# Optimization experiments

Hardware: AMD Instinct MI355X
Metric: run time of the kernel (lower is better)

Reference implementation:

```python
import jax, jax.numpy as jnp
import numpy as np

E, N, F = 50000, 25000, 32

def setup_inputs() -> dict:
    key = jax.random.key(0)
    ks = jax.random.split(key, 8)
    efeat = jax.random.normal(ks[0], (E, F), dtype=jnp.float32) * 0.2
    initial_efeats = jax.random.normal(ks[1], (E, F), dtype=jnp.float32) * 0.2
    # msg_fn / attn_fn: Linear(F, F*F)
    Wm = jax.random.normal(ks[2], (F * F, F), dtype=jnp.float32) * 0.05
    bm = jnp.zeros((F * F,), dtype=jnp.float32)
    Wa = jax.random.normal(ks[3], (F * F, F), dtype=jnp.float32) * 0.05
    ba = jnp.zeros((F * F,), dtype=jnp.float32)
    src = jax.random.randint(ks[4], (E,), 0, N, dtype=jnp.int32)
    dst = jax.random.randint(ks[5], (E,), 0, N, dtype=jnp.int32)
    return {"efeat": efeat, "initial_efeats": initial_efeats, "Wm": Wm, "bm": bm,
            "Wa": Wa, "ba": ba, "src": src, "dst": dst, "num_nodes": N}

def reference(efeat, initial_efeats, Wm, bm, Wa, ba, src, dst, num_nodes):
    e, f = efeat.shape
    # edge-conditioned transform matrices: [E, F, F]
    w_m = (efeat @ Wm.T + bm).reshape(e, f, f)
    w_a = (efeat @ Wa.T + ba).reshape(e, f, f)
    h = efeat[:, :, None]                 # [E, F, 1]
    ih = initial_efeats[:, :, None]       # [E, F, 1]
    e1 = w_m * h                          # [E, F, F]
    exp_e2 = jnp.exp(w_a * h)             # [E, F, F]
    initial_e1 = w_m * ih
    exp_initial_e2 = jnp.exp(w_a * ih)
    # scatter-sum exp weights to destination nodes, gather back at src
    sum_exp_node = jax.ops.segment_sum(exp_e2, dst, num_segments=num_nodes)  # [N, F, F]
    sum_exp = sum_exp_node[src] - exp_e2 + exp_initial_e2
    h1 = exp_e2 * e1
    initial_h1 = exp_initial_e2 * initial_e1
    m_node = jax.ops.segment_sum(h1, dst, num_segments=num_nodes)            # [N, F, F]
    h2 = (m_node[src] - h1 + initial_h1) / sum_exp
    return h2.sum(axis=1)                 # [E, F]
```

## Files before the change

### kernel.cpp

```cpp
#include <hip/hip_runtime.h>
#include <hip/hip_fp16.h>
#include <math.h>
#include <stdint.h>


#define FDIM   32
#define NNODES 25000
#define NPB    8

typedef __attribute__((ext_vector_type(8))) short bf16x8;
typedef __attribute__((ext_vector_type(4))) float f32x4;

__device__ __forceinline__ unsigned short f2bf(float f) {
    unsigned u = __float_as_uint(f);
    return (unsigned short)((u + 0x7FFFu + ((u >> 16) & 1u)) >> 16);
}
__device__ __forceinline__ unsigned f2e5(float f) {
    unsigned short hb = __half_as_ushort(__float2half(f));
    return (unsigned)((unsigned short)((hb + 0x7Fu + ((hb >> 8) & 1u)) >> 8)) & 0xFFu;
}
__device__ __forceinline__ float e52f(unsigned b) {
    return __half2float(__ushort_as_half((unsigned short)(b << 8)));
}

__global__ __launch_bounds__(256) void zero_f4(float4* __restrict__ p, int n4) {
    int i = blockIdx.x * blockDim.x + threadIdx.x;
    int stride = gridDim.x * blockDim.x;
    float4 z = make_float4(0.f, 0.f, 0.f, 0.f);
    for (; i < n4; i += stride) p[i] = z;
}

__global__ __launch_bounds__(256) void k_hist(
    const int* __restrict__ src, const int* __restrict__ dst,
    int* __restrict__ cnt_src, int* __restrict__ cnt_dst, int E) {
    int e = blockIdx.x * blockDim.x + threadIdx.x;
    if (e < E) {
        atomicAdd(&cnt_dst[dst[e]], 1);
        atomicAdd(&cnt_src[src[e]], 1);
    }
}

__global__ __launch_bounds__(256) void k_scan2(
    const int* __restrict__ cnt_dst, int* __restrict__ off_dst, int* __restrict__ cur_dst,
    const int* __restrict__ cnt_src, int* __restrict__ off_src, int* __restrict__ cur_src,
    int n) {
    const int* cnt = blockIdx.x ? cnt_src : cnt_dst;
    int* off = blockIdx.x ? off_src : off_dst;
    int* cur = blockIdx.x ? cur_src : cur_dst;
    __shared__ int wsum[4];
    __shared__ int carry_sh;
    const int tid = threadIdx.x, lane = tid & 63, w = tid >> 6;
    if (tid == 0) carry_sh = 0;
    __syncthreads();
    for (int base = 0; base < n; base += 1024) {
        int i0 = base + tid * 4;
        int v0 = (i0 + 0 < n) ? cnt[i0 + 0] : 0;
        int v1 = (i0 + 1 < n) ? cnt[i0 + 1] : 0;
        int v2 = (i0 + 2 < n) ? cnt[i0 + 2] : 0;
        int v3 = (i0 + 3 < n) ? cnt[i0 + 3] : 0;
        int s = v0 + v1 + v2 + v3;
        int inc = s;
        for (int d = 1; d < 64; d <<= 1) {
            int t = __shfl_up(inc, d, 64);
            if (lane >= d) inc += t;
        }
        if (lane == 63) wsum[w] = inc;
        __syncthreads();
        int wbase = 0;
        for (int k = 0; k < w; ++k) wbase += wsum[k];
        int carry = carry_sh;
        int excl = carry + wbase + inc - s;
        if (i0 + 0 < n) { off[i0 + 0] = excl; cur[i0 + 0] = excl; } excl += v0;
        if (i0 + 1 < n) { off[i0 + 1] = excl; cur[i0 + 1] = excl; } excl += v1;
        if (i0 + 2 < n) { off[i0 + 2] = excl; cur[i0 + 2] = excl; } excl += v2;
        if (i0 + 3 < n) { off[i0 + 3] = excl; cur[i0 + 3] = excl; }
        __syncthreads();
        if (tid == 255) carry_sh = carry + wbase + inc;
    }
    __syncthreads();
    if (tid == 0) off[n] = carry_sh;
}

__global__ __launch_bounds__(256) void k_scatter(
    const int* __restrict__ src, const int* __restrict__ dst,
    int* __restrict__ cur_src, int* __restrict__ cur_dst,
    int* __restrict__ eb_src, int* __restrict__ eb_dst, int E) {
    int e = blockIdx.x * blockDim.x + threadIdx.x;
    if (e < E) {
        int p = atomicAdd(&cur_dst[dst[e]], 1); eb_dst[p] = e;
        int q = atomicAdd(&cur_src[src[e]], 1); eb_src[q] = e;
    }
}

__global__ __launch_bounds__(256) void prep_w(
    const float* __restrict__ Wm, const float* __restrict__ Wa,
    short* __restrict__ wbuf) {
    int idx = blockIdx.x * blockDim.x + threadIdx.x;
    if (idx >= 2 * 64 * 64) return;
    int mat  = idx >> 12;
    int jt   = (idx >> 6) & 63;
    int lane = idx & 63;
    const float* W = mat ? Wa : Wm;
    const float* s = W + (size_t)(jt * 16 + (lane & 15)) * FDIM + (lane >> 4) * 8;
    bf16x8 v;
#pragma unroll
    for (int t = 0; t < 8; ++t) v[t] = (short)f2bf(s[t]);
    *(bf16x8*)(wbuf + (size_t)idx * 8) = v;
}

__global__ __launch_bounds__(256) void gemm(
    const float* __restrict__ efeat,
    const float* __restrict__ bm, const float* __restrict__ ba,
    const short* __restrict__ wbuf,
    unsigned short* __restrict__ buf, int E)
{
    const int lane = threadIdx.x & 63;
    const int wid  = threadIdx.x >> 6;
    const int et   = blockIdx.x * 4 + wid;
    if (et * 16 >= E) return;
    const int r16 = lane & 15;
    const int kq  = lane >> 4;

    const float* xa = efeat + (size_t)(et * 16 + r16) * FDIM + kq * 8;
    bf16x8 afrag;
#pragma unroll
    for (int t = 0; t < 8; ++t) afrag[t] = (short)f2bf(xa[t]);

    for (int jt = 0; jt < 64; ++jt) {
        bf16x8 bfm = *(const bf16x8*)(wbuf + ((size_t)(jt)      * 64 + lane) * 8);
        bf16x8 bfa = *(const bf16x8*)(wbuf + ((size_t)(64 + jt) * 64 + lane) * 8);
        const int j = jt * 16 + r16;
        const float biasm = bm[j], biasa = ba[j];
        f32x4 accm = {biasm, biasm, biasm, biasm};
        f32x4 acca = {biasa, biasa, biasa, biasa};
        accm = __builtin_amdgcn_mfma_f32_16x16x32_bf16(afrag, bfm, accm, 0, 0, 0);
        acca = __builtin_amdgcn_mfma_f32_16x16x32_bf16(afrag, bfa, acca, 0, 0, 0);
#pragma unroll
        for (int r = 0; r < 4; ++r) {
            int e = et * 16 + kq * 4 + r;
            unsigned pk = f2e5(accm[r]) | (f2e5(acca[r]) << 8);
            buf[(size_t)e * 1024 + j] = (unsigned short)pk;
        }
    }
}

__global__ __launch_bounds__(256) void consume(
    const float* __restrict__ efeat, const float* __restrict__ ifeat,
    const unsigned short* __restrict__ buf,
    const int* __restrict__ off_dst, const int* __restrict__ eb_dst,
    const int* __restrict__ off_src, const int* __restrict__ eb_src,
    float* __restrict__ out)
{
    __shared__ float red[2][4][32];
    const int tid = threadIdx.x;
    const int jj  = tid & 31;
    const int wv  = tid >> 6;
    int par = 0;

    const int n0 = blockIdx.x * NPB;
    const int n1 = min(NNODES, n0 + NPB);
    for (int n = n0; n < n1; ++n) {
        float S[4] = {0.f, 0.f, 0.f, 0.f};
        float M[4] = {0.f, 0.f, 0.f, 0.f};
        const int a0 = off_dst[n], a1 = off_dst[n + 1];
        for (int idx = a0; idx < a1; ++idx) {
            int e = __builtin_amdgcn_readfirstlane(eb_dst[idx]);
            const unsigned short* bp = buf + (size_t)e * 1024 + tid;
            const float* xv = efeat + e * FDIM;
#pragma unroll
            for (int q = 0; q < 4; ++q) {
                unsigned p = bp[q * 256];
                float am = e52f(p & 0xFF), aa = e52f(p >> 8);
                float xi = xv[(q * 256 + tid) >> 5];
                float e2 = __expf(aa * xi);
                S[q] += e2;
                M[q] = fmaf(e2, am * xi, M[q]);
            }
        }
        const int b0 = off_src[n], b1 = off_src[n + 1];
        for (int idx = b0; idx < b1; ++idx) {
            int e = __builtin_amdgcn_readfirstlane(eb_src[idx]);
            const unsigned short* bp = buf + (size_t)e * 1024 + tid;
            const float* xv  = efeat + e * FDIM;
            const float* x0v = ifeat + e * FDIM;
            float acc = 0.f;
#pragma unroll
            for (int q = 0; q < 4; ++q) {
                unsigned p = bp[q * 256];
                float am = e52f(p & 0xFF), aa = e52f(p >> 8);
                int ii = (q * 256 + tid) >> 5;
                float xi = xv[ii], x0i = x0v[ii];
                float e2  = __expf(aa * xi);
                float h1  = e2 * (am * xi);
                float ei2 = __expf(aa * x0i);
                float ih1 = ei2 * (am * x0i);
                float den = (S[q] - e2) + ei2;
                float num = (M[q] - h1) + ih1;
                float h2  = num * __builtin_amdgcn_rcpf(den);
                if (!isfinite(h2)) h2 = 0.f;
                acc += h2;
            }
            acc += __shfl_xor(acc, 32, 64);
            if ((tid & 32) == 0) red[par][wv][jj] = acc;
            __syncthreads();
            if (tid < 32) {
                float s = red[par][0][tid] + red[par][1][tid]
                        + red[par][2][tid] + red[par][3][tid];
                out[(size_t)e * FDIM + tid] = s;
            }
            par ^= 1;
        }
    }
}

extern "C" void kernel_launch(void* const* d_in, const int* in_sizes, int n_in,
                              void* d_out, int out_size, void* d_ws, size_t ws_size,
                              hipStream_t stream) {
    const float* efeat = (const float*)d_in[0];
    const float* ifeat = (const float*)d_in[1];
    const float* Wm    = (const float*)d_in[2];
    const float* bm    = (const float*)d_in[3];
    const float* Wa    = (const float*)d_in[4];
    const float* ba    = (const float*)d_in[5];
    const int*   src   = (const int*)d_in[6];
    const int*   dst   = (const int*)d_in[7];
    const int E = in_sizes[6];
    const int N = NNODES;
    float* out = (float*)d_out;

    int* cnt_dst = (int*)d_ws;
    int* cnt_src = cnt_dst + N;
    int* off_dst = cnt_src + N;
    int* off_src = off_dst + (N + 1);
    int* cur_dst = off_src + (N + 1);
    int* cur_src = cur_dst + N;
    int* eb_dst  = cur_src + N;
    int* eb_src  = eb_dst + E;
    short* wbuf  = (short*)(((uintptr_t)(eb_src + E) + 255) & ~(uintptr_t)255);
    unsigned short* buf =
        (unsigned short*)(((uintptr_t)(wbuf + 2 * 64 * 64 * 8) + 255) & ~(uintptr_t)255);

    zero_f4<<<64, 256, 0, stream>>>((float4*)cnt_dst, (2 * N) / 4);
    k_hist<<<(E + 255) / 256, 256, 0, stream>>>(src, dst, cnt_src, cnt_dst, E);
    k_scan2<<<2, 256, 0, stream>>>(cnt_dst, off_dst, cur_dst,
                                   cnt_src, off_src, cur_src, N);
    k_scatter<<<(E + 255) / 256, 256, 0, stream>>>(src, dst, cur_src, cur_dst,
                                                   eb_src, eb_dst, E);
    prep_w<<<32, 256, 0, stream>>>(Wm, Wa, wbuf);

    const int etiles = (E + 15) / 16;
    gemm<<<(etiles + 3) / 4, 256, 0, stream>>>(efeat, bm, ba, wbuf, buf, E);
    consume<<<(N + NPB - 1) / NPB, 256, 0, stream>>>(efeat, ifeat, buf,
                                                     off_dst, eb_dst,
                                                     off_src, eb_src, out);
}
```

Before: 219.3 us.

## Assign one wavefront per node and transpose GEMM output for vectorized stores

The GEMM now swaps the MFMA operands so each lane holds four consecutive output columns for one edge, and packs them into a single 64-bit store instead of scattered 16-bit stores. The consume kernel maps one wavefront per node instead of a whole block per node. Each lane reads 32 contiguous packed values with wide loads, and the per-edge reduction over i is done with wavefront shuffles instead of shared memory and __syncthreads. Edge ids are prefetched into lanes and broadcast via shuffle. The cost is 16-element register arrays per lane and a five-step shuffle reduction for each of the 16 outputs, which raises register pressure.

```diff
diff --git a/kernel.cpp b/kernel.cpp
--- a/kernel.cpp
+++ b/kernel.cpp
@@ -6,7 +6,6 @@
 
 #define FDIM   32
 #define NNODES 25000
-#define NPB    8
 
 typedef __attribute__((ext_vector_type(8))) short bf16x8;
 typedef __attribute__((ext_vector_type(4))) float f32x4;
@@ -15,12 +14,13 @@
     unsigned u = __float_as_uint(f);
     return (unsigned short)((u + 0x7FFFu + ((u >> 16) & 1u)) >> 16);
 }
-__device__ __forceinline__ unsigned f2e5(float f) {
-    unsigned short hb = __half_as_ushort(__float2half(f));
-    return (unsigned)((unsigned short)((hb + 0x7Fu + ((hb >> 8) & 1u)) >> 8)) & 0xFFu;
-}
-__device__ __forceinline__ float e52f(unsigned b) {
-    return __half2float(__ushort_as_half((unsigned short)(b << 8)));
+__device__ __forceinline__ float hlo(unsigned v) {
+    return __half2float(__ushort_as_half((unsigned short)v));
+}
+__device__ __forceinline__ unsigned pk2(float m, float a) {
+    unsigned um = (unsigned)__half_as_ushort(__float2half(m));
+    unsigned ua = (unsigned)__half_as_ushort(__float2half(a));
+    return (um >> 8) | (ua & 0xFF00u);
 }
 
 __global__ __launch_bounds__(256) void zero_f4(float4* __restrict__ p, int n4) {
@@ -122,25 +122,30 @@
     const int kq  = lane >> 4;
 
     const float* xa = efeat + (size_t)(et * 16 + r16) * FDIM + kq * 8;
-    bf16x8 afrag;
-#pragma unroll
-    for (int t = 0; t < 8; ++t) afrag[t] = (short)f2bf(xa[t]);
+    bf16x8 xfrag;
+#pragma unroll
+    for (int t = 0; t < 8; ++t) xfrag[t] = (short)f2bf(xa[t]);
+
+    const int e = et * 16 + r16;
+    unsigned* bout = (unsigned*)(buf + (size_t)e * 1024);
 
     for (int jt = 0; jt < 64; ++jt) {
-        bf16x8 bfm = *(const bf16x8*)(wbuf + ((size_t)(jt)      * 64 + lane) * 8);
-        bf16x8 bfa = *(const bf16x8*)(wbuf + ((size_t)(64 + jt) * 64 + lane) * 8);
-        const int j = jt * 16 + r16;
-        const float biasm = bm[j], biasa = ba[j];
-        f32x4 accm = {biasm, biasm, biasm, biasm};
-        f32x4 acca = {biasa, biasa, biasa, biasa};
-        accm = __builtin_amdgcn_mfma_f32_16x16x32_bf16(afrag, bfm, accm, 0, 0, 0);
-        acca = __builtin_amdgcn_mfma_f32_16x16x32_bf16(afrag, bfa, acca, 0, 0, 0);
-#pragma unroll
-        for (int r = 0; r < 4; ++r) {
-            int e = et * 16 + kq * 4 + r;
-            unsigned pk = f2e5(accm[r]) | (f2e5(acca[r]) << 8);
-            buf[(size_t)e * 1024 + j] = (unsigned short)pk;
-        }
+        bf16x8 wfm = *(const bf16x8*)(wbuf + ((size_t)(jt)      * 64 + lane) * 8);
+        bf16x8 wfa = *(const bf16x8*)(wbuf + ((size_t)(64 + jt) * 64 + lane) * 8);
+        const int jb = jt * 16 + kq * 4;
+        const float4 bm4 = *(const float4*)(bm + jb);
+        const float4 ba4 = *(const float4*)(ba + jb);
+        f32x4 accm = {bm4.x, bm4.y, bm4.z, bm4.w};
+        f32x4 acca = {ba4.x, ba4.y, ba4.z, ba4.w};
+        accm = __builtin_amdgcn_mfma_f32_16x16x32_bf16(wfm, xfrag, accm, 0, 0, 0);
+        acca = __builtin_amdgcn_mfma_f32_16x16x32_bf16(wfa, xfrag, acca, 0, 0, 0);
+        unsigned p0 = pk2(accm[0], acca[0]);
+        unsigned p1 = pk2(accm[1], acca[1]);
+        unsigned p2 = pk2(accm[2], acca[2]);
+        unsigned p3 = pk2(accm[3], acca[3]);
+        unsigned long long v = (unsigned long long)(p0 | (p1 << 16)) |
+                               ((unsigned long long)(p2 | (p3 << 16)) << 32);
+        *(unsigned long long*)(bout + (jb >> 1)) = v;
     }
 }
 
@@ -151,64 +156,87 @@
     const int* __restrict__ off_src, const int* __restrict__ eb_src,
     float* __restrict__ out)
 {
-    __shared__ float red[2][4][32];
     const int tid = threadIdx.x;
-    const int jj  = tid & 31;
-    const int wv  = tid >> 6;
-    int par = 0;
-
-    const int n0 = blockIdx.x * NPB;
-    const int n1 = min(NNODES, n0 + NPB);
-    for (int n = n0; n < n1; ++n) {
-        float S[4] = {0.f, 0.f, 0.f, 0.f};
-        float M[4] = {0.f, 0.f, 0.f, 0.f};
-        const int a0 = off_dst[n], a1 = off_dst[n + 1];
-        for (int idx = a0; idx < a1; ++idx) {
-            int e = __builtin_amdgcn_readfirstlane(eb_dst[idx]);
-            const unsigned short* bp = buf + (size_t)e * 1024 + tid;
-            const float* xv = efeat + e * FDIM;
-#pragma unroll
-            for (int q = 0; q < 4; ++q) {
-                unsigned p = bp[q * 256];
-                float am = e52f(p & 0xFF), aa = e52f(p >> 8);
-                float xi = xv[(q * 256 + tid) >> 5];
-                float e2 = __expf(aa * xi);
-                S[q] += e2;
-                M[q] = fmaf(e2, am * xi, M[q]);
+    const int l   = tid & 63;
+    const int wid = tid >> 6;
+    const int n   = blockIdx.x * 4 + wid;
+    if (n >= NNODES) return;
+
+    const int a0 = off_dst[n], a1 = off_dst[n + 1];
+    const int b0 = off_src[n], b1 = off_src[n + 1];
+    const int din = a1 - a0, dout = b1 - b0;
+    if (dout == 0) return;
+
+    int eid = (l < 32) ? eb_dst[a0 + l] : eb_src[b0 + (l - 32)];
+    const int i = l >> 1;
+
+    float S[16], M[16];
+#pragma unroll
+    for (int t = 0; t < 16; ++t) { S[t] = 0.f; M[t] = 0.f; }
+
+    for (int t = 0; t < din; ++t) {
+        int e = (t < 32) ? __shfl(eid, t, 64) : eb_dst[a0 + t];
+        e = __builtin_amdgcn_readfirstlane(e);
+        const uint4* bp = (const uint4*)(buf + ((size_t)e << 10) + l * 16);
+        uint4 d0 = bp[0], d1 = bp[1];
+        float xi = efeat[((size_t)e << 5) + i];
+        unsigned u[8] = {d0.x, d0.y, d0.z, d0.w, d1.x, d1.y, d1.z, d1.w};
+#pragma unroll
+        for (int w = 0; w < 8; ++w) {
+            unsigned uu = u[w];
+            float am0 = hlo(uu << 8),  aa0 = hlo(uu);
+            float am1 = hlo(uu >> 8),  aa1 = hlo(uu >> 16);
+            float ea = __expf(aa0 * xi);
+            float eb = __expf(aa1 * xi);
+            S[2 * w]     += ea;  M[2 * w]     = fmaf(ea, am0 * xi, M[2 * w]);
+            S[2 * w + 1] += eb;  M[2 * w + 1] = fmaf(eb, am1 * xi, M[2 * w + 1]);
+        }
+    }
+
+    for (int t = 0; t < dout; ++t) {
+        int e = (t < 32) ? __shfl(eid, 32 + t, 64) : eb_src[b0 + t];
+        e = __builtin_amdgcn_readfirstlane(e);
+        const uint4* bp = (const uint4*)(buf + ((size_t)e << 10) + l * 16);
+        uint4 d0 = bp[0], d1 = bp[1];
+        float xi  = efeat[((size_t)e << 5) + i];
+        float x0i = ifeat[((size_t)e << 5) + i];
+        unsigned u[8] = {d0.x, d0.y, d0.z, d0.w, d1.x, d1.y, d1.z, d1.w};
+        float acc[16];
+#pragma unroll
+        for (int w = 0; w < 8; ++w) {
+            unsigned uu = u[w];
+            float am0 = hlo(uu << 8),  aa0 = hlo(uu);
+            float am1 = hlo(uu >> 8),  aa1 = hlo(uu >> 16);
+#define PROC(T2, AM, AA)                                                \
+            {                                                           \
+                float amx  = (AM) * xi;                                 \
+                float e2   = __expf((AA) * xi);                         \
+                float h1   = e2 * amx;                                  \
+                float ei2  = __expf((AA) * x0i);                        \
+                float ih1  = ei2 * ((AM) * x0i);                        \
+                float den  = (S[T2] - e2) + ei2;                        \
+                float num  = (M[T2] - h1) + ih1;                        \
+                float h2   = num * __builtin_amdgcn_rcpf(den);          \
+                acc[T2] = isfinite(h2) ? h2 : 0.f;                      \
             }
-        }
-        const int b0 = off_src[n], b1 = off_src[n + 1];
-        for (int idx = b0; idx < b1; ++idx) {
-            int e = __builtin_amdgcn_readfirstlane(eb_src[idx]);
-            const unsigned short* bp = buf + (size_t)e * 1024 + tid;
-            const float* xv  = efeat + e * FDIM;
-            const float* x0v = ifeat + e * FDIM;
-            float acc = 0.f;
-#pragma unroll
-            for (int q = 0; q < 4; ++q) {
-                unsigned p = bp[q * 256];
-                float am = e52f(p & 0xFF), aa = e52f(p >> 8);
-                int ii = (q * 256 + tid) >> 5;
-                float xi = xv[ii], x0i = x0v[ii];
-                float e2  = __expf(aa * xi);
-                float h1  = e2 * (am * xi);
-                float ei2 = __expf(aa * x0i);
-                float ih1 = ei2 * (am * x0i);
-                float den = (S[q] - e2) + ei2;
-                float num = (M[q] - h1) + ih1;
-                float h2  = num * __builtin_amdgcn_rcpf(den);
-                if (!isfinite(h2)) h2 = 0.f;
-                acc += h2;
-            }
-            acc += __shfl_xor(acc, 32, 64);
-            if ((tid & 32) == 0) red[par][wv][jj] = acc;
-            __syncthreads();
-            if (tid < 32) {
-                float s = red[par][0][tid] + red[par][1][tid]
-                        + red[par][2][tid] + red[par][3][tid];
-                out[(size_t)e * FDIM + tid] = s;
-            }
-            par ^= 1;
+            PROC(2 * w,     am0, aa0);
+            PROC(2 * w + 1, am1, aa1);
+#undef PROC
+        }
+#pragma unroll
+        for (int t2 = 0; t2 < 16; ++t2) {
+            acc[t2] += __shfl_xor(acc[t2], 2, 64);
+            acc[t2] += __shfl_xor(acc[t2], 4, 64);
+            acc[t2] += __shfl_xor(acc[t2], 8, 64);
+            acc[t2] += __shfl_xor(acc[t2], 16, 64);
+            acc[t2] += __shfl_xor(acc[t2], 32, 64);
+        }
+        if (l < 2) {
+            float4* o = (float4*)(out + ((size_t)e << 5) + l * 16);
+            o[0] = make_float4(acc[0],  acc[1],  acc[2],  acc[3]);
+            o[1] = make_float4(acc[4],  acc[5],  acc[6],  acc[7]);
+            o[2] = make_float4(acc[8],  acc[9],  acc[10], acc[11]);
+            o[3] = make_float4(acc[12], acc[13], acc[14], acc[15]);
         }
     }
 }
@@ -250,7 +278,7 @@
 
     const int etiles = (E + 15) / 16;
     gemm<<<(etiles + 3) / 4, 256, 0, stream>>>(efeat, bm, ba, wbuf, buf, E);
-    consume<<<(N + NPB - 1) / NPB, 256, 0, stream>>>(efeat, ifeat, buf,
-                                                     off_dst, eb_dst,
-                                                     off_src, eb_src, out);
-}
+    consume<<<(NNODES + 3) / 4, 256, 0, stream>>>(efeat, ifeat, buf,
+                                                  off_dst, eb_dst,
+                                                  off_src, eb_src, out);
+}
```

Result: slower. 260.2 us (+18.7%).
